# Kernel optimization log

Measured on AMD Instinct MI355X. Metric: run time of the kernel, lower is better.

## Reference

```python
import jax, jax.numpy as jnp
import numpy as np


def setup_inputs() -> dict:
    key = jax.random.key(0)
    k1, k2, k3 = jax.random.split(key, 3)
    B, A, CI, CO, E = 2048, 128, 128, 128, 4
    x = jax.random.normal(k1, (B, A, CI), dtype=jnp.float32)
    atom_numbers = jax.random.randint(k2, (B, A), 0, 9, dtype=jnp.int32)
    # glorot-uniform-ish init for W; zeros for b (matches model_ops.zeros)
    limit = np.sqrt(6.0 / (CI + CO)).astype(np.float32)
    W = jax.random.uniform(k3, (E, CI, CO), dtype=jnp.float32, minval=-limit, maxval=limit)
    b = jnp.zeros((E, CO), dtype=jnp.float32)
    atom_cases = jnp.array([1, 6, 7, 8], dtype=jnp.int32)
    return {"x": x, "atom_numbers": atom_numbers, "W": W, "b": b, "atom_cases": atom_cases}


def reference(x, atom_numbers, W, b, atom_cases):
    # Per-expert dense: h[e,b,a,o] = relu(x[b,a,:] @ W[e] + b[e])
    h = jax.nn.relu(jnp.einsum('bai,eio->ebao', x, W) + b[:, None, None, :])
    # mask[e,b,a] = 1 where atom_numbers == atom_cases[e]
    mask = (atom_numbers[None, :, :] == atom_cases[:, None, None]).astype(x.dtype)
    # masked sum over experts -> [B, max_atoms, out_channels]
    return jnp.einsum('ebao,eba->bao', h, mask)
```

## Files before the change

### kernel.cpp

```cpp
#include <hip/hip_runtime.h>
#include <hip/hip_bf16.h>
#include <stdint.h>


typedef __attribute__((ext_vector_type(8))) short short8;
typedef __attribute__((ext_vector_type(4))) float f32x4;

#define NROWS 262144
#define PERM_OFF 16

__device__ __forceinline__ unsigned short f2bf(float f) {
    union { float f; uint32_t u; } v; v.f = f;
    uint32_t u = v.u;
    return (unsigned short)((u + 0x7FFFu + ((u >> 16) & 1u)) >> 16);
}

__global__ void k0_zero(uint32_t* __restrict__ ws) {
    if (threadIdx.x < 16) ws[threadIdx.x] = 0u;
}

__device__ __forceinline__ int bucket_of(int v, int c0, int c1, int c2, int c3) {
    return (v == c0) ? 0 : (v == c1) ? 1 : (v == c2) ? 2 : (v == c3) ? 3 : 4;
}

__global__ __launch_bounds__(256) void k1_count(const int* __restrict__ an,
                                                const int* __restrict__ cases,
                                                uint32_t* __restrict__ ws) {
    __shared__ uint32_t lc[5];
    if (threadIdx.x < 5) lc[threadIdx.x] = 0u;
    __syncthreads();
    const int c0 = cases[0], c1 = cases[1], c2 = cases[2], c3 = cases[3];
    const int r0 = (blockIdx.x * 256 + threadIdx.x) * 4;
    const int4 a = *(const int4*)(an + r0);
    atomicAdd(&lc[bucket_of(a.x, c0, c1, c2, c3)], 1u);
    atomicAdd(&lc[bucket_of(a.y, c0, c1, c2, c3)], 1u);
    atomicAdd(&lc[bucket_of(a.z, c0, c1, c2, c3)], 1u);
    atomicAdd(&lc[bucket_of(a.w, c0, c1, c2, c3)], 1u);
    __syncthreads();
    if (threadIdx.x < 5) atomicAdd(&ws[threadIdx.x], lc[threadIdx.x]);
}

__global__ void k2_prefix(uint32_t* __restrict__ ws) {
    if (threadIdx.x == 0) {
        uint32_t run = 0;
        #pragma unroll
        for (int b = 0; b < 5; ++b) {
            ws[5 + b]  = run;
            ws[10 + b] = run;
            run += ws[b];
        }
    }
}

__global__ __launch_bounds__(256) void k3_scatter(const int* __restrict__ an,
                                                  const int* __restrict__ cases,
                                                  uint32_t* __restrict__ ws) {
    __shared__ uint32_t lc[5];
    __shared__ uint32_t lbase[5];
    if (threadIdx.x < 5) lc[threadIdx.x] = 0u;
    __syncthreads();
    const int c0 = cases[0], c1 = cases[1], c2 = cases[2], c3 = cases[3];
    const int r0 = (blockIdx.x * 256 + threadIdx.x) * 4;
    const int4 a = *(const int4*)(an + r0);
    int bk[4];
    bk[0] = bucket_of(a.x, c0, c1, c2, c3);
    bk[1] = bucket_of(a.y, c0, c1, c2, c3);
    bk[2] = bucket_of(a.z, c0, c1, c2, c3);
    bk[3] = bucket_of(a.w, c0, c1, c2, c3);
    uint32_t slot[4];
    #pragma unroll
    for (int i = 0; i < 4; ++i) slot[i] = atomicAdd(&lc[bk[i]], 1u);
    __syncthreads();
    if (threadIdx.x < 5) lbase[threadIdx.x] = atomicAdd(&ws[10 + threadIdx.x], lc[threadIdx.x]);
    __syncthreads();
    uint32_t* __restrict__ perm = ws + PERM_OFF;
    #pragma unroll
    for (int i = 0; i < 4; ++i) perm[lbase[bk[i]] + slot[i]] = (uint32_t)(r0 + i);
}

__global__ __launch_bounds__(512, 4) void k4_gemm(const float* __restrict__ x,
                                                  const float* __restrict__ W,
                                                  const float* __restrict__ bvec,
                                                  const uint32_t* __restrict__ ws,
                                                  float* __restrict__ out) {
    __shared__ unsigned short Wlds[16384];
    __shared__ int ridx[128];

    int b = -1, chunk = 0, accb = 0;
    #pragma unroll
    for (int bb = 0; bb < 5; ++bb) {
        const int nb = (int)((ws[bb] + 127u) >> 7);
        if (b < 0 && (int)blockIdx.x < accb + nb) { b = bb; chunk = blockIdx.x - accb; }
        accb += nb;
    }
    if (b < 0) return;

    const int cb   = (int)ws[b];
    const int rbeg = chunk << 7;
    const int nval = min(128, cb - rbeg);
    const uint32_t* __restrict__ perm = ws + PERM_OFF;
    if (threadIdx.x < 128)
        ridx[threadIdx.x] = (threadIdx.x < nval)
                          ? (int)perm[ws[5 + b] + rbeg + threadIdx.x] : -1;

    const int lane = threadIdx.x & 63;
    const int wv   = threadIdx.x >> 6;

    if (b == 4) {
        __syncthreads();
        const int half = lane >> 5;
        const int l32  = lane & 31;
        const float4 z = make_float4(0.f, 0.f, 0.f, 0.f);
        #pragma unroll
        for (int it = 0; it < 8; ++it) {
            const int r = ridx[wv * 16 + it * 2 + half];
            if (r >= 0) *(float4*)(out + (size_t)r * 128 + l32 * 4) = z;
        }
        return;
    }

    for (int idx = threadIdx.x; idx < 16384; idx += 512) {
        const int col = idx & 15;
        const int j   = (idx >> 4) & 7;
        const int gg  = (idx >> 7) & 3;
        const int nt  = (idx >> 9) & 7;
        const int kk  = (idx >> 12) & 3;
        const int k   = kk * 32 + gg * 8 + j;
        const float w = W[(size_t)(b * 128 + k) * 128 + nt * 16 + col];
        Wlds[((kk * 8 + nt) * 64 + gg * 16 + col) * 8 + j] = f2bf(w);
    }
    __syncthreads();

    const int g4  = lane >> 4;
    const int c16 = lane & 15;
    const int rg  = wv >> 2;
    const int ng  = wv & 3;

    const float bv0 = bvec[b * 128 + (ng * 2 + 0) * 16 + c16];
    const float bv1 = bvec[b * 128 + (ng * 2 + 1) * 16 + c16];

    int arow[4];
    #pragma unroll
    for (int mf = 0; mf < 4; ++mf) arow[mf] = ridx[rg * 64 + mf * 16 + c16];

    f32x4 acc[4][2];
    #pragma unroll
    for (int mf = 0; mf < 4; ++mf) {
        acc[mf][0] = (f32x4){0.f, 0.f, 0.f, 0.f};
        acc[mf][1] = (f32x4){0.f, 0.f, 0.f, 0.f};
    }

    const short8* __restrict__ Wfrag = (const short8*)Wlds;

    #pragma unroll
    for (int kk = 0; kk < 4; ++kk) {
        short8 afr[4];
        #pragma unroll
        for (int mf = 0; mf < 4; ++mf) {
            float4 fa = make_float4(0.f, 0.f, 0.f, 0.f);
            float4 fb = make_float4(0.f, 0.f, 0.f, 0.f);
            if (arow[mf] >= 0) {
                const float* p = x + (size_t)arow[mf] * 128 + kk * 32 + g4 * 8;
                fa = *(const float4*)p;
                fb = *(const float4*)(p + 4);
            }
            short8 a;
            a[0] = (short)f2bf(fa.x); a[1] = (short)f2bf(fa.y);
            a[2] = (short)f2bf(fa.z); a[3] = (short)f2bf(fa.w);
            a[4] = (short)f2bf(fb.x); a[5] = (short)f2bf(fb.y);
            a[6] = (short)f2bf(fb.z); a[7] = (short)f2bf(fb.w);
            afr[mf] = a;
        }
        const short8 b0 = Wfrag[(kk * 8 + ng * 2 + 0) * 64 + lane];
        const short8 b1 = Wfrag[(kk * 8 + ng * 2 + 1) * 64 + lane];
        #pragma unroll
        for (int mf = 0; mf < 4; ++mf) {
            acc[mf][0] = __builtin_amdgcn_mfma_f32_16x16x32_bf16(afr[mf], b0, acc[mf][0], 0, 0, 0);
            acc[mf][1] = __builtin_amdgcn_mfma_f32_16x16x32_bf16(afr[mf], b1, acc[mf][1], 0, 0, 0);
        }
    }

    #pragma unroll
    for (int mf = 0; mf < 4; ++mf) {
        #pragma unroll
        for (int r = 0; r < 4; ++r) {
            const int orow = ridx[rg * 64 + mf * 16 + g4 * 4 + r];
            if (orow >= 0) {
                out[(size_t)orow * 128 + (ng * 2 + 0) * 16 + c16] = fmaxf(acc[mf][0][r] + bv0, 0.f);
                out[(size_t)orow * 128 + (ng * 2 + 1) * 16 + c16] = fmaxf(acc[mf][1][r] + bv1, 0.f);
            }
        }
    }
}

extern "C" void kernel_launch(void* const* d_in, const int* in_sizes, int n_in,
                              void* d_out, int out_size, void* d_ws, size_t ws_size,
                              hipStream_t stream) {
    const float* x     = (const float*)d_in[0];
    const int*   an    = (const int*)d_in[1];
    const float* W     = (const float*)d_in[2];
    const float* bvec  = (const float*)d_in[3];
    const int*   cases = (const int*)d_in[4];
    float*    out = (float*)d_out;
    uint32_t* ws  = (uint32_t*)d_ws;

    k0_zero   <<<1,    64,  0, stream>>>(ws);
    k1_count  <<<256,  256, 0, stream>>>(an, cases, ws);
    k2_prefix <<<1,    64,  0, stream>>>(ws);
    k3_scatter<<<256,  256, 0, stream>>>(an, cases, ws);
    k4_gemm   <<<2053, 512, 0, stream>>>(x, W, bvec, ws, out);
}
```

Measured before the change: 259.7 us.

## Drop count/prefix kernels, prepack W to bf16 once, stage output via LDS

Removes the count and prefix kernels by giving each bucket a fixed-capacity region in the permutation buffer, so one scatter pass suffices. W is converted to bf16 in MFMA fragment layout once, in a small prep kernel, and the GEMM loads fragments from global memory instead of every block rebuilding them in LDS. Outputs are staged through padded LDS so each row is written with coalesced float4 stores, and fp32-to-bf16 packing uses the paired conversion intrinsic. The risks are a larger workspace footprint, an extra LDS buffer that can lower occupancy, and a grid size of 2052 that must still cover every bucket.

```diff
diff --git a/kernel.cpp b/kernel.cpp
--- a/kernel.cpp
+++ b/kernel.cpp
@@ -6,57 +6,46 @@
 typedef __attribute__((ext_vector_type(8))) short short8;
 typedef __attribute__((ext_vector_type(4))) float f32x4;
 
-#define NROWS 262144
-#define PERM_OFF 16
+#define PERM_U32_OFF 65536
+#define BUCKET_CAP   262144
+#define OST_STRIDE   132
 
-__device__ __forceinline__ unsigned short f2bf(float f) {
-    union { float f; uint32_t u; } v; v.f = f;
-    uint32_t u = v.u;
-    return (unsigned short)((u + 0x7FFFu + ((u >> 16) & 1u)) >> 16);
-}
-
-__global__ void k0_zero(uint32_t* __restrict__ ws) {
-    if (threadIdx.x < 16) ws[threadIdx.x] = 0u;
-}
+union U16 { uint4 u; short8 s; };
 
 __device__ __forceinline__ int bucket_of(int v, int c0, int c1, int c2, int c3) {
     return (v == c0) ? 0 : (v == c1) ? 1 : (v == c2) ? 2 : (v == c3) ? 3 : 4;
 }
 
-__global__ __launch_bounds__(256) void k1_count(const int* __restrict__ an,
-                                                const int* __restrict__ cases,
-                                                uint32_t* __restrict__ ws) {
-    __shared__ uint32_t lc[5];
-    if (threadIdx.x < 5) lc[threadIdx.x] = 0u;
-    __syncthreads();
-    const int c0 = cases[0], c1 = cases[1], c2 = cases[2], c3 = cases[3];
-    const int r0 = (blockIdx.x * 256 + threadIdx.x) * 4;
-    const int4 a = *(const int4*)(an + r0);
-    atomicAdd(&lc[bucket_of(a.x, c0, c1, c2, c3)], 1u);
-    atomicAdd(&lc[bucket_of(a.y, c0, c1, c2, c3)], 1u);
-    atomicAdd(&lc[bucket_of(a.z, c0, c1, c2, c3)], 1u);
-    atomicAdd(&lc[bucket_of(a.w, c0, c1, c2, c3)], 1u);
-    __syncthreads();
-    if (threadIdx.x < 5) atomicAdd(&ws[threadIdx.x], lc[threadIdx.x]);
+__device__ __forceinline__ uint32_t pkbf(float lo, float hi) {
+    __hip_bfloat162 h = __float22bfloat162_rn(make_float2(lo, hi));
+    uint32_t r;
+    __builtin_memcpy(&r, &h, 4);
+    return r;
 }
 
-__global__ void k2_prefix(uint32_t* __restrict__ ws) {
-    if (threadIdx.x == 0) {
-        uint32_t run = 0;
-        #pragma unroll
-        for (int b = 0; b < 5; ++b) {
-            ws[5 + b]  = run;
-            ws[10 + b] = run;
-            run += ws[b];
-        }
-    }
+__global__ __launch_bounds__(256) void k_prep(const float* __restrict__ W,
+                                              uint32_t* __restrict__ ws) {
+    if (blockIdx.x == 0 && threadIdx.x < 8) ws[threadIdx.x] = 0u;
+    const int T   = blockIdx.x * 256 + threadIdx.x;
+    const int c16 = T & 15;
+    const int g   = (T >> 4) & 3;
+    const int nt  = (T >> 6) & 7;
+    const int kk  = (T >> 9) & 3;
+    const int e   = (T >> 11) & 3;
+    float v[8];
+    #pragma unroll
+    for (int j = 0; j < 8; ++j)
+        v[j] = W[(size_t)(e * 128 + kk * 32 + g * 8 + j) * 128 + nt * 16 + c16];
+    uint4 pack = make_uint4(pkbf(v[0], v[1]), pkbf(v[2], v[3]),
+                            pkbf(v[4], v[5]), pkbf(v[6], v[7]));
+    const int lane = g * 16 + c16;
+    *(uint4*)((char*)ws + 1024 + e * 32768 + ((kk * 8 + nt) * 64 + lane) * 16) = pack;
 }
 
-__global__ __launch_bounds__(256) void k3_scatter(const int* __restrict__ an,
-                                                  const int* __restrict__ cases,
-                                                  uint32_t* __restrict__ ws) {
-    __shared__ uint32_t lc[5];
-    __shared__ uint32_t lbase[5];
+__global__ __launch_bounds__(256) void k_scatter(const int* __restrict__ an,
+                                                 const int* __restrict__ cases,
+                                                 uint32_t* __restrict__ ws) {
+    __shared__ uint32_t lc[5], lbase[5];
     if (threadIdx.x < 5) lc[threadIdx.x] = 0u;
     __syncthreads();
     const int c0 = cases[0], c1 = cases[1], c2 = cases[2], c3 = cases[3];
@@ -71,20 +60,20 @@
     #pragma unroll
     for (int i = 0; i < 4; ++i) slot[i] = atomicAdd(&lc[bk[i]], 1u);
     __syncthreads();
-    if (threadIdx.x < 5) lbase[threadIdx.x] = atomicAdd(&ws[10 + threadIdx.x], lc[threadIdx.x]);
+    if (threadIdx.x < 5) lbase[threadIdx.x] = atomicAdd(&ws[threadIdx.x], lc[threadIdx.x]);
     __syncthreads();
-    uint32_t* __restrict__ perm = ws + PERM_OFF;
+    uint32_t* __restrict__ perm = ws + PERM_U32_OFF;
     #pragma unroll
-    for (int i = 0; i < 4; ++i) perm[lbase[bk[i]] + slot[i]] = (uint32_t)(r0 + i);
+    for (int i = 0; i < 4; ++i)
+        perm[bk[i] * BUCKET_CAP + lbase[bk[i]] + slot[i]] = (uint32_t)(r0 + i);
 }
 
-__global__ __launch_bounds__(512, 4) void k4_gemm(const float* __restrict__ x,
-                                                  const float* __restrict__ W,
-                                                  const float* __restrict__ bvec,
-                                                  const uint32_t* __restrict__ ws,
-                                                  float* __restrict__ out) {
-    __shared__ unsigned short Wlds[16384];
-    __shared__ int ridx[128];
+__global__ __launch_bounds__(512, 4) void k_gemm(const float* __restrict__ x,
+                                                 const float* __restrict__ bvec,
+                                                 const uint32_t* __restrict__ ws,
+                                                 float* __restrict__ out) {
+    __shared__ int   ridx[128];
+    __shared__ float ost[128 * OST_STRIDE];
 
     int b = -1, chunk = 0, accb = 0;
     #pragma unroll
@@ -98,18 +87,16 @@
     const int cb   = (int)ws[b];
     const int rbeg = chunk << 7;
     const int nval = min(128, cb - rbeg);
-    const uint32_t* __restrict__ perm = ws + PERM_OFF;
+    const uint32_t* __restrict__ perm = ws + PERM_U32_OFF + (size_t)b * BUCKET_CAP;
     if (threadIdx.x < 128)
-        ridx[threadIdx.x] = (threadIdx.x < nval)
-                          ? (int)perm[ws[5 + b] + rbeg + threadIdx.x] : -1;
+        ridx[threadIdx.x] = (threadIdx.x < nval) ? (int)perm[rbeg + threadIdx.x] : -1;
+    __syncthreads();
 
     const int lane = threadIdx.x & 63;
     const int wv   = threadIdx.x >> 6;
 
     if (b == 4) {
-        __syncthreads();
-        const int half = lane >> 5;
-        const int l32  = lane & 31;
+        const int half = lane >> 5, l32 = lane & 31;
         const float4 z = make_float4(0.f, 0.f, 0.f, 0.f);
         #pragma unroll
         for (int it = 0; it < 8; ++it) {
@@ -118,18 +105,6 @@
         }
         return;
     }
-
-    for (int idx = threadIdx.x; idx < 16384; idx += 512) {
-        const int col = idx & 15;
-        const int j   = (idx >> 4) & 7;
-        const int gg  = (idx >> 7) & 3;
-        const int nt  = (idx >> 9) & 7;
-        const int kk  = (idx >> 12) & 3;
-        const int k   = kk * 32 + gg * 8 + j;
-        const float w = W[(size_t)(b * 128 + k) * 128 + nt * 16 + col];
-        Wlds[((kk * 8 + nt) * 64 + gg * 16 + col) * 8 + j] = f2bf(w);
-    }
-    __syncthreads();
 
     const int g4  = lane >> 4;
     const int c16 = lane & 15;
@@ -150,10 +125,13 @@
         acc[mf][1] = (f32x4){0.f, 0.f, 0.f, 0.f};
     }
 
-    const short8* __restrict__ Wfrag = (const short8*)Wlds;
+    const uint4* __restrict__ wf = (const uint4*)((const char*)ws + 1024 + b * 32768);
 
     #pragma unroll
     for (int kk = 0; kk < 4; ++kk) {
+        U16 wb0, wb1;
+        wb0.u = wf[(kk * 8 + ng * 2 + 0) * 64 + lane];
+        wb1.u = wf[(kk * 8 + ng * 2 + 1) * 64 + lane];
         short8 afr[4];
         #pragma unroll
         for (int mf = 0; mf < 4; ++mf) {
@@ -164,19 +142,15 @@
                 fa = *(const float4*)p;
                 fb = *(const float4*)(p + 4);
             }
-            short8 a;
-            a[0] = (short)f2bf(fa.x); a[1] = (short)f2bf(fa.y);
-            a[2] = (short)f2bf(fa.z); a[3] = (short)f2bf(fa.w);
-            a[4] = (short)f2bf(fb.x); a[5] = (short)f2bf(fb.y);
-            a[6] = (short)f2bf(fb.z); a[7] = (short)f2bf(fb.w);
-            afr[mf] = a;
+            U16 av;
+            av.u = make_uint4(pkbf(fa.x, fa.y), pkbf(fa.z, fa.w),
+                              pkbf(fb.x, fb.y), pkbf(fb.z, fb.w));
+            afr[mf] = av.s;
         }
-        const short8 b0 = Wfrag[(kk * 8 + ng * 2 + 0) * 64 + lane];
-        const short8 b1 = Wfrag[(kk * 8 + ng * 2 + 1) * 64 + lane];
         #pragma unroll
         for (int mf = 0; mf < 4; ++mf) {
-            acc[mf][0] = __builtin_amdgcn_mfma_f32_16x16x32_bf16(afr[mf], b0, acc[mf][0], 0, 0, 0);
-            acc[mf][1] = __builtin_amdgcn_mfma_f32_16x16x32_bf16(afr[mf], b1, acc[mf][1], 0, 0, 0);
+            acc[mf][0] = __builtin_amdgcn_mfma_f32_16x16x32_bf16(afr[mf], wb0.s, acc[mf][0], 0, 0, 0);
+            acc[mf][1] = __builtin_amdgcn_mfma_f32_16x16x32_bf16(afr[mf], wb1.s, acc[mf][1], 0, 0, 0);
         }
     }
 
@@ -184,11 +158,21 @@
     for (int mf = 0; mf < 4; ++mf) {
         #pragma unroll
         for (int r = 0; r < 4; ++r) {
-            const int orow = ridx[rg * 64 + mf * 16 + g4 * 4 + r];
-            if (orow >= 0) {
-                out[(size_t)orow * 128 + (ng * 2 + 0) * 16 + c16] = fmaxf(acc[mf][0][r] + bv0, 0.f);
-                out[(size_t)orow * 128 + (ng * 2 + 1) * 16 + c16] = fmaxf(acc[mf][1][r] + bv1, 0.f);
-            }
+            const int row = rg * 64 + mf * 16 + g4 * 4 + r;
+            ost[row * OST_STRIDE + (ng * 2 + 0) * 16 + c16] = fmaxf(acc[mf][0][r] + bv0, 0.f);
+            ost[row * OST_STRIDE + (ng * 2 + 1) * 16 + c16] = fmaxf(acc[mf][1][r] + bv1, 0.f);
+        }
+    }
+    __syncthreads();
+
+    const int l32 = lane & 31, lh = lane >> 5;
+    #pragma unroll
+    for (int i = 0; i < 8; ++i) {
+        const int row  = wv * 16 + i * 2 + lh;
+        const int orow = ridx[row];
+        if (orow >= 0) {
+            const float4 vv = *(const float4*)&ost[row * OST_STRIDE + l32 * 4];
+            *(float4*)(out + (size_t)orow * 128 + l32 * 4) = vv;
         }
     }
 }
@@ -204,9 +188,7 @@
     float*    out = (float*)d_out;
     uint32_t* ws  = (uint32_t*)d_ws;
 
-    k0_zero   <<<1,    64,  0, stream>>>(ws);
-    k1_count  <<<256,  256, 0, stream>>>(an, cases, ws);
-    k2_prefix <<<1,    64,  0, stream>>>(ws);
-    k3_scatter<<<256,  256, 0, stream>>>(an, cases, ws);
-    k4_gemm   <<<2053, 512, 0, stream>>>(x, W, bvec, ws, out);
+    k_prep   <<<32,   256, 0, stream>>>(W, ws);
+    k_scatter<<<256,  256, 0, stream>>>(an, cases, ws);
+    k_gemm   <<<2052, 512, 0, stream>>>(x, bvec, ws, out);
 }
```

Measured after the change: 242.7 us. 6.5% less time.
